# Optimization experiments

Hardware: AMD Instinct MI355X
Metric: run time of the kernel (lower is better)

The kernel has to match this reference:

```python
import jax, jax.numpy as jnp
import numpy as np

B, S, H, HKV, D, BS = 2, 2048, 32, 8, 128, 16
HIDDEN = H * D            # 4096
G = H // HKV              # 4 query heads per kv head
NB = S // BS              # 128 blocks per sequence
SCALE = D ** -0.5


def setup_inputs() -> dict:
    key = jax.random.key(0)
    k1, k2, k3 = jax.random.split(key, 3)
    T = B * S
    hidden_states = jax.random.normal(k1, (T, HIDDEN), dtype=jnp.float32)
    w_qkv = jax.random.normal(k2, (HIDDEN, HIDDEN + 2 * HKV * D), dtype=jnp.float32) * 0.02
    w_out = jax.random.normal(k3, (HIDDEN, HIDDEN), dtype=jnp.float32) * 0.02
    k_cache = jnp.zeros((B * NB, HKV, BS, D), dtype=jnp.float32)
    v_cache = jnp.zeros((B * NB, HKV, BS, D), dtype=jnp.float32)
    block_tables = jnp.arange(B * NB, dtype=jnp.int32).reshape(B, NB)
    return {"hidden_states": hidden_states, "w_qkv": w_qkv, "w_out": w_out,
            "k_cache": k_cache, "v_cache": v_cache, "block_tables": block_tables}


def reference(hidden_states, w_qkv, w_out, k_cache, v_cache, block_tables):
    # qkv projection on packed tokens [T, hidden]
    qkv = hidden_states @ w_qkv
    q, k, v = jnp.split(qkv, [HIDDEN, HIDDEN + HKV * D], axis=-1)
    q = q.reshape(B, S, H, D)
    k = k.reshape(B, S, HKV, D)
    v = v.reshape(B, S, HKV, D)

    # --- paged KV store: scatter per-block pages into cache via block_tables ---
    # [B, NB, BS, HKV, D] -> page layout [B, NB, HKV, BS, D]
    k_pages = k.reshape(B, NB, BS, HKV, D).transpose(0, 1, 3, 2, 4)
    v_pages = v.reshape(B, NB, BS, HKV, D).transpose(0, 1, 3, 2, 4)
    k_cache = k_cache.at[block_tables].set(k_pages)
    v_cache = v_cache.at[block_tables].set(v_pages)

    # --- paged KV gather for prefill attention ---
    kg = k_cache[block_tables].transpose(0, 2, 1, 3, 4).reshape(B, HKV, S, D)
    vg = v_cache[block_tables].transpose(0, 2, 1, 3, 4).reshape(B, HKV, S, D)

    # GQA causal attention: group query heads per kv head
    qh = q.transpose(0, 2, 1, 3).reshape(B, HKV, G, S, D)
    scores = jnp.einsum('bhgqd,bhkd->bhgqk', qh, kg) * SCALE
    causal = jnp.tril(jnp.ones((S, S), dtype=bool))
    scores = jnp.where(causal, scores, -jnp.inf)
    attn = jax.nn.softmax(scores, axis=-1)
    out = jnp.einsum('bhgqk,bhkd->bhgqd', attn, vg)   # [B,HKV,G,S,D]
    out = out.reshape(B, H, S, D).transpose(0, 2, 1, 3).reshape(B * S, HIDDEN)
    return out @ w_out
```

## Files before the change

### kernel.cpp

```cpp
#include <hip/hip_runtime.h>

#define BB 2
#define SS 2048
#define HH 32
#define HKV 8
#define DD 128
#define HIDDEN 4096
#define NQK 6144
#define TT 4096
#define SCALE 0.08838834764831843f
#define SCALE_LOG2E 0.12751743444f

typedef __attribute__((ext_vector_type(8), __may_alias__)) short short8;
typedef __attribute__((ext_vector_type(4), __may_alias__)) short short4v;
typedef __attribute__((ext_vector_type(4), __may_alias__)) float floatx4;

__device__ __forceinline__ short f2bf(float x) {
    unsigned u = __builtin_bit_cast(unsigned, x);
    u += 0x7FFFu + ((u >> 16) & 1u);
    return (short)(u >> 16);
}

__device__ __forceinline__ void gload_lds16(const short* g, short* l) {
    __builtin_amdgcn_global_load_lds((const __attribute__((address_space(1))) void*)g,
                                     (__attribute__((address_space(3))) void*)l, 16, 0, 0);
}

__global__ __launch_bounds__(256) void cvt_f32_bf16(const float* __restrict__ src,
                                                    short* __restrict__ dst) {
    int i = blockIdx.x * 256 + threadIdx.x;
    typedef __attribute__((ext_vector_type(4), __may_alias__)) float f4;
    f4 v = ((const f4*)src)[i];
    short4v o = { f2bf(v.x), f2bf(v.y), f2bf(v.z), f2bf(v.w) };
    ((short4v*)dst)[i] = o;
}

__global__ __launch_bounds__(256) void transpose_cvt(const float* __restrict__ src,
                                                     short* __restrict__ dst,
                                                     int rows, int cols) {
    __shared__ float t[32][33];
    int tx = threadIdx.x, ty = threadIdx.y;
    int c0 = blockIdx.x * 32, r0 = blockIdx.y * 32;
#pragma unroll
    for (int i = 0; i < 32; i += 8) t[ty + i][tx] = src[(size_t)(r0 + ty + i) * cols + c0 + tx];
    __syncthreads();
#pragma unroll
    for (int i = 0; i < 32; i += 8)
        dst[(size_t)(c0 + ty + i) * rows + r0 + tx] = f2bf(t[tx][ty + i]);
}

__global__ __launch_bounds__(256) void build_vt(const short* __restrict__ qkv,
                                                short* __restrict__ vt) {
    __shared__ short t[32][33];
    int tx = threadIdx.x, ty = threadIdx.y;
    int s0 = blockIdx.x * 32, d0 = blockIdx.y * 32;
    int bh = blockIdx.z; int b = bh >> 3, hk = bh & 7;
#pragma unroll
    for (int i = 0; i < 32; i += 8)
        t[ty + i][tx] = qkv[(size_t)(b * SS + s0 + ty + i) * NQK + 5120 + hk * DD + d0 + tx];
    __syncthreads();
#pragma unroll
    for (int i = 0; i < 32; i += 8)
        vt[(size_t)(bh * DD + d0 + ty + i) * SS + s0 + tx] = t[tx][ty + i];
}

template <int OUT_BF16>
__global__ __launch_bounds__(512, 2) void gemm_bt(const short* __restrict__ A,
                                                  const short* __restrict__ Bt,
                                                  void* __restrict__ Cout,
                                                  int M, int N, int K) {
    (void)M;
    __shared__ __align__(16) short smem[65536];
    const int tid  = threadIdx.x;
    const int wave = tid >> 6, lane = tid & 63;
    const int qn = lane & 15, quad = lane >> 4;
    const int wm = wave >> 2, wn = wave & 3;

    int bid = blockIdx.y * gridDim.x + blockIdx.x;
    int xcd = bid & 7, idx = bid >> 3;
    int bnx = gridDim.x >> 2;
    int xm = xcd & 1, xn = xcd >> 1;
    int im = idx & 7, in_ = idx >> 3;
    const int m0 = (xm * 8 + im) * 256;
    const int n0 = (xn * bnx + in_) * 256;

    const int NT = K >> 6;

    const int srow = tid >> 3;
    const int scg  = (tid & 7) ^ (srow & 7);
    const short* aS = A  + (size_t)(m0 + srow) * K + scg * 8;
    const short* bS = Bt + (size_t)(n0 + srow) * K + scg * 8;
    const int lwo = wave * 512;

#define STAGE_A(buf, blk, tt) gload_lds16(aS + (size_t)(blk) * 64 * K + (size_t)(tt) * 64, \
                                          smem + (buf) + (blk) * 4096 + lwo)
#define STAGE_B(buf, blk, tt) gload_lds16(bS + (size_t)(blk) * 64 * K + (size_t)(tt) * 64, \
                                          smem + (buf) + 16384 + (blk) * 4096 + lwo)

    const int xorm  = (qn & 7) << 3;
    const int a_row = (wm * 128 + qn) * 64;
    const int b_row = (wn * 64 + qn) * 64;
    const int col0  = (quad * 8) ^ xorm;
    const int col1  = col0 ^ 32;

#pragma unroll
    for (int blk = 0; blk < 4; blk++) { STAGE_A(0, blk, 0); STAGE_B(0, blk, 0); }
    if (NT > 1) {
#pragma unroll
        for (int blk = 0; blk < 4; blk++) { STAGE_A(32768, blk, 1); STAGE_B(32768, blk, 1); }
        asm volatile("s_waitcnt vmcnt(8)" ::: "memory");
    } else {
        asm volatile("s_waitcnt vmcnt(0)" ::: "memory");
    }
    __builtin_amdgcn_s_barrier();

    floatx4 acc[8][4] = {};

#pragma unroll 2
    for (int t = 0; t < NT; ++t) {
        const int cb = (t & 1) << 15;
        const short* Ab = smem + cb;
        const short* Bb = smem + cb + 16384;
        short8 a[4][2], b0[2][2], b1[2][2], a2[4][2];

#pragma unroll
        for (int mt = 0; mt < 4; mt++) {
            a[mt][0] = *(const short8*)(Ab + a_row + mt * 1024 + col0);
            a[mt][1] = *(const short8*)(Ab + a_row + mt * 1024 + col1);
        }
#pragma unroll
        for (int nt = 0; nt < 2; nt++) {
            b0[nt][0] = *(const short8*)(Bb + b_row + nt * 1024 + col0);
            b0[nt][1] = *(const short8*)(Bb + b_row + nt * 1024 + col1);
        }
        asm volatile("s_waitcnt lgkmcnt(8)" ::: "memory");
        __builtin_amdgcn_s_barrier();
        asm volatile("s_waitcnt lgkmcnt(0)" ::: "memory");
        __builtin_amdgcn_s_setprio(1);
#pragma unroll
        for (int mt = 0; mt < 4; mt++)
#pragma unroll
            for (int nt = 0; nt < 2; nt++) {
                acc[mt][nt] = __builtin_amdgcn_mfma_f32_16x16x32_bf16(a[mt][0], b0[nt][0], acc[mt][nt], 0, 0, 0);
                acc[mt][nt] = __builtin_amdgcn_mfma_f32_16x16x32_bf16(a[mt][1], b0[nt][1], acc[mt][nt], 0, 0, 0);
            }
        __builtin_amdgcn_s_setprio(0);
        __builtin_amdgcn_s_barrier();

#pragma unroll
        for (int nt = 0; nt < 2; nt++) {
            b1[nt][0] = *(const short8*)(Bb + b_row + 2048 + nt * 1024 + col0);
            b1[nt][1] = *(const short8*)(Bb + b_row + 2048 + nt * 1024 + col1);
        }
        if (t + 2 < NT) { STAGE_A(cb, 0, t + 2); STAGE_A(cb, 2, t + 2); }
        __builtin_amdgcn_s_barrier();
        asm volatile("s_waitcnt lgkmcnt(0)" ::: "memory");
        __builtin_amdgcn_s_setprio(1);
#pragma unroll
        for (int mt = 0; mt < 4; mt++)
#pragma unroll
            for (int nt = 0; nt < 2; nt++) {
                acc[mt][2 + nt] = __builtin_amdgcn_mfma_f32_16x16x32_bf16(a[mt][0], b1[nt][0], acc[mt][2 + nt], 0, 0, 0);
                acc[mt][2 + nt] = __builtin_amdgcn_mfma_f32_16x16x32_bf16(a[mt][1], b1[nt][1], acc[mt][2 + nt], 0, 0, 0);
            }
        __builtin_amdgcn_s_setprio(0);
        __builtin_amdgcn_s_barrier();

#pragma unroll
        for (int mt = 0; mt < 4; mt++) {
            a2[mt][0] = *(const short8*)(Ab + 4096 + a_row + mt * 1024 + col0);
            a2[mt][1] = *(const short8*)(Ab + 4096 + a_row + mt * 1024 + col1);
        }
        if (t + 2 < NT) { STAGE_B(cb, 0, t + 2); STAGE_B(cb, 1, t + 2);
                          STAGE_B(cb, 2, t + 2); STAGE_B(cb, 3, t + 2); }
        __builtin_amdgcn_s_barrier();
        asm volatile("s_waitcnt lgkmcnt(0)" ::: "memory");
        __builtin_amdgcn_s_setprio(1);
#pragma unroll
        for (int mt = 0; mt < 4; mt++)
#pragma unroll
            for (int nt = 0; nt < 2; nt++) {
                acc[4 + mt][2 + nt] = __builtin_amdgcn_mfma_f32_16x16x32_bf16(a2[mt][0], b1[nt][0], acc[4 + mt][2 + nt], 0, 0, 0);
                acc[4 + mt][2 + nt] = __builtin_amdgcn_mfma_f32_16x16x32_bf16(a2[mt][1], b1[nt][1], acc[4 + mt][2 + nt], 0, 0, 0);
            }
        __builtin_amdgcn_s_setprio(0);
        __builtin_amdgcn_s_barrier();

        if (t + 2 < NT) { STAGE_A(cb, 1, t + 2); STAGE_A(cb, 3, t + 2); }
        __builtin_amdgcn_s_setprio(1);
#pragma unroll
        for (int mt = 0; mt < 4; mt++)
#pragma unroll
            for (int nt = 0; nt < 2; nt++) {
                acc[4 + mt][nt] = __builtin_amdgcn_mfma_f32_16x16x32_bf16(a2[mt][0], b0[nt][0], acc[4 + mt][nt], 0, 0, 0);
                acc[4 + mt][nt] = __builtin_amdgcn_mfma_f32_16x16x32_bf16(a2[mt][1], b0[nt][1], acc[4 + mt][nt], 0, 0, 0);
            }
        __builtin_amdgcn_s_setprio(0);
        if (t + 2 < NT) asm volatile("s_waitcnt vmcnt(8)" ::: "memory");
        else            asm volatile("s_waitcnt vmcnt(0)" ::: "memory");
        __builtin_amdgcn_s_barrier();
    }
#undef STAGE_A
#undef STAGE_B

    const int erow = m0 + wm * 128 + quad * 4;
    const int ecol = n0 + wn * 64 + qn;
#pragma unroll
    for (int mt = 0; mt < 8; mt++)
#pragma unroll
        for (int nt = 0; nt < 4; nt++)
#pragma unroll
            for (int r = 0; r < 4; r++) {
                size_t off = (size_t)(erow + mt * 16 + r) * N + ecol + nt * 16;
                if (OUT_BF16) ((short*)Cout)[off] = f2bf(acc[mt][nt][r]);
                else          ((float*)Cout)[off] = acc[mt][nt][r];
            }
}

__global__ __launch_bounds__(256) void attn_kernel(const short* __restrict__ qkv,
                                                   const short* __restrict__ vt,
                                                   short* __restrict__ out) {
    __shared__ __align__(16) short Kb[2 * 64 * 128];
    __shared__ __align__(16) short Vb[2 * 128 * 64];
    __shared__ __align__(16) short Ps[4 * 32 * 40];
    int tid = threadIdx.x, wave = tid >> 6, lane = tid & 63;
    int qn = lane & 15, quad = lane >> 4;
    int bid = blockIdx.x;
    int qt = 63 - (bid >> 4);
    int b  = (bid >> 3) & 1;
    int hk = bid & 7;
    int qb = qt * 32;
    int h  = hk * 4 + wave;
    int bh = b * 8 + hk;

    short8 qf[2][4];
#pragma unroll
    for (int nt = 0; nt < 2; nt++) {
        const short* qrow = qkv + (size_t)(b * SS + qb + nt * 16 + qn) * NQK + h * DD;
#pragma unroll
        for (int c = 0; c < 4; c++) qf[nt][c] = *(const short8*)(qrow + c * 32 + quad * 8);
    }
    const short8 onesv = { 0x3F80, 0x3F80, 0x3F80, 0x3F80, 0x3F80, 0x3F80, 0x3F80, 0x3F80 };
    floatx4 oacc[8][2] = {};
    floatx4 lacc[2] = {};
    const int nmac = (qt + 2) >> 1;

    const int kRow = tid >> 4;
    const int kCgp = (tid & 15) ^ (kRow & 7);
    const int vRow = tid >> 3;
    const int vCgp = (tid & 7) ^ (vRow & 7);
    const short* kSrc = qkv + (size_t)(b * SS) * NQK + HIDDEN + hk * DD + kCgp * 8;
    const short* vSrc = vt + (size_t)(bh * DD) * SS + vCgp * 8;
    short* kDst = Kb + wave * 512;
    short* vDst = Vb + wave * 512;

#define STAGEKV(buf, kb) do {                                                          \
    _Pragma("unroll")                                                                  \
    for (int c = 0; c < 4; c++)                                                        \
        gload_lds16(kSrc + (size_t)((kb) + c * 16 + kRow) * NQK,                       \
                    kDst + (buf) * 8192 + c * 2048);                                   \
    _Pragma("unroll")                                                                  \
    for (int c = 0; c < 4; c++)                                                        \
        gload_lds16(vSrc + (size_t)(c * 32 + vRow) * SS + (kb),                        \
                    vDst + (buf) * 8192 + c * 2048);                                   \
    } while (0)

    STAGEKV(0, 0);
    __syncthreads();

    const int kxor = (qn & 7) * 8;

    for (int it = 0; it < nmac; ++it) {
        const int cur = it & 1;
        if (it + 1 < nmac) STAGEKV(cur ^ 1, (it + 1) * 64);
        const short* Kc = Kb + cur * 8192;
        const short* Vc = Vb + cur * 8192;

#pragma unroll
        for (int s = 0; s < 2; ++s) {
            const int kb_s = it * 64 + s * 32;
            if (kb_s > qb) break;
            const bool needMask = (kb_s == qb);

            floatx4 sc[2][2] = {};
#pragma unroll
            for (int c = 0; c < 4; c++) {
                int cg = ((c * 4 + quad) * 8) ^ kxor;
                short8 k0 = *(const short8*)(Kc + (s * 32 + qn) * 128 + cg);
                short8 k1 = *(const short8*)(Kc + (s * 32 + 16 + qn) * 128 + cg);
#pragma unroll
                for (int nt = 0; nt < 2; nt++) {
                    sc[0][nt] = __builtin_amdgcn_mfma_f32_16x16x32_bf16(k0, qf[nt][c], sc[0][nt], 0, 0, 0);
                    sc[1][nt] = __builtin_amdgcn_mfma_f32_16x16x32_bf16(k1, qf[nt][c], sc[1][nt], 0, 0, 0);
                }
            }

            short* pw = Ps + wave * (32 * 40);
#pragma unroll
            for (int nt = 0; nt < 2; nt++)
#pragma unroll
                for (int kt = 0; kt < 2; kt++) {
                    float e[4];
#pragma unroll
                    for (int r = 0; r < 4; r++) {
                        float v = exp2f(sc[kt][nt][r] * SCALE_LOG2E);
                        bool masked = needMask && (kb_s + kt * 16 + quad * 4 + r > qb + nt * 16 + qn);
                        e[r] = masked ? 0.f : v;
                    }
                    short4v pk = { f2bf(e[0]), f2bf(e[1]), f2bf(e[2]), f2bf(e[3]) };
                    *(short4v*)(pw + (nt * 16 + qn) * 40 + kt * 16 + quad * 4) = pk;
                }
            short8 pf[2];
#pragma unroll
            for (int nt = 0; nt < 2; nt++)
                pf[nt] = *(const short8*)(pw + (nt * 16 + qn) * 40 + quad * 8);

            __builtin_amdgcn_s_setprio(1);
#pragma unroll
            for (int dt = 0; dt < 8; dt++) {
                short8 vf = *(const short8*)(Vc + (dt * 16 + qn) * 64 + ((((s << 2) + quad) * 8) ^ kxor));
#pragma unroll
                for (int nt = 0; nt < 2; nt++)
                    oacc[dt][nt] = __builtin_amdgcn_mfma_f32_16x16x32_bf16(vf, pf[nt], oacc[dt][nt], 0, 0, 0);
            }
#pragma unroll
            for (int nt = 0; nt < 2; nt++)
                lacc[nt] = __builtin_amdgcn_mfma_f32_16x16x32_bf16(onesv, pf[nt], lacc[nt], 0, 0, 0);
            __builtin_amdgcn_s_setprio(0);
        }
        __syncthreads();
    }
#undef STAGEKV

#pragma unroll
    for (int nt = 0; nt < 2; nt++) {
        float inv = 1.0f / lacc[nt][0];
        short* orow = out + (size_t)(b * SS + qb + nt * 16 + qn) * HIDDEN + h * DD;
#pragma unroll
        for (int dt = 0; dt < 8; dt++) {
            short4v ov = { f2bf(oacc[dt][nt][0] * inv), f2bf(oacc[dt][nt][1] * inv),
                           f2bf(oacc[dt][nt][2] * inv), f2bf(oacc[dt][nt][3] * inv) };
            *(short4v*)(orow + dt * 16 + quad * 4) = ov;
        }
    }
}

extern "C" void kernel_launch(void* const* d_in, const int* in_sizes, int n_in,
                              void* d_out, int out_size, void* d_ws, size_t ws_size,
                              hipStream_t stream) {
    (void)in_sizes; (void)n_in; (void)out_size; (void)ws_size;
    const float* hs    = (const float*)d_in[0];
    const float* w_qkv = (const float*)d_in[1];
    const float* w_out = (const float*)d_in[2];

    char* ws = (char*)d_ws;
    short* hsb   = (short*)(ws);
    short* wqkvT = (short*)(ws + 33554432);
    short* woutT = (short*)(ws + 83886080);
    short* qkv   = (short*)(ws + 117440512);
    short* vtb   = (short*)(ws + 167772160);
    short* attnb = (short*)(ws + 176160768);

    cvt_f32_bf16<<<16384, 256, 0, stream>>>(hs, hsb);
    transpose_cvt<<<dim3(192, 128), dim3(32, 8), 0, stream>>>(w_qkv, wqkvT, HIDDEN, NQK);
    transpose_cvt<<<dim3(128, 128), dim3(32, 8), 0, stream>>>(w_out, woutT, HIDDEN, HIDDEN);
    gemm_bt<1><<<dim3(NQK / 256, TT / 256), 512, 0, stream>>>(hsb, wqkvT, qkv, TT, NQK, HIDDEN);
    build_vt<<<dim3(64, 4, 16), dim3(32, 8), 0, stream>>>(qkv, vtb);
    attn_kernel<<<1024, 256, 0, stream>>>(qkv, vtb, attnb);
    gemm_bt<0><<<dim3(HIDDEN / 256, TT / 256), 512, 0, stream>>>(attnb, woutT, d_out, TT, HIDDEN, HIDDEN);
}
```

Before: 734.7 us.

## Split attention query rows across 8 waves and vectorize weight transpose

The attention kernel now launches 512 threads per block. Each wave handles 16 query rows of one head instead of 32, so there are 8 waves. KV tiles shrink from 64 to 32 keys, each tile is staged with one LDS load per thread, and the swizzle is reworked to match. The goal is more waves per CU and fewer live registers per wave, at the cost of more barrier iterations over a smaller tile. Separately, the weight transpose-convert kernel uses 64x64 tiles with float4 loads and 16-byte bf16 stores to cut memory transactions.

```diff
diff --git a/kernel.cpp b/kernel.cpp
--- a/kernel.cpp
+++ b/kernel.cpp
@@ -14,6 +14,7 @@
 typedef __attribute__((ext_vector_type(8), __may_alias__)) short short8;
 typedef __attribute__((ext_vector_type(4), __may_alias__)) short short4v;
 typedef __attribute__((ext_vector_type(4), __may_alias__)) float floatx4;
+typedef __attribute__((ext_vector_type(4), __may_alias__)) float f4;
 
 __device__ __forceinline__ short f2bf(float x) {
     unsigned u = __builtin_bit_cast(unsigned, x);
@@ -29,7 +30,6 @@
 __global__ __launch_bounds__(256) void cvt_f32_bf16(const float* __restrict__ src,
                                                     short* __restrict__ dst) {
     int i = blockIdx.x * 256 + threadIdx.x;
-    typedef __attribute__((ext_vector_type(4), __may_alias__)) float f4;
     f4 v = ((const f4*)src)[i];
     short4v o = { f2bf(v.x), f2bf(v.y), f2bf(v.z), f2bf(v.w) };
     ((short4v*)dst)[i] = o;
@@ -38,15 +38,27 @@
 __global__ __launch_bounds__(256) void transpose_cvt(const float* __restrict__ src,
                                                      short* __restrict__ dst,
                                                      int rows, int cols) {
-    __shared__ float t[32][33];
-    int tx = threadIdx.x, ty = threadIdx.y;
-    int c0 = blockIdx.x * 32, r0 = blockIdx.y * 32;
-#pragma unroll
-    for (int i = 0; i < 32; i += 8) t[ty + i][tx] = src[(size_t)(r0 + ty + i) * cols + c0 + tx];
+    __shared__ float t[64][65];
+    int c0 = blockIdx.x * 64, r0 = blockIdx.y * 64;
+    int tx = threadIdx.x & 15, ty = threadIdx.x >> 4;
+#pragma unroll
+    for (int i = 0; i < 64; i += 16) {
+        f4 v = *(const f4*)(src + (size_t)(r0 + ty + i) * cols + c0 + tx * 4);
+        t[ty + i][tx * 4 + 0] = v.x;
+        t[ty + i][tx * 4 + 1] = v.y;
+        t[ty + i][tx * 4 + 2] = v.z;
+        t[ty + i][tx * 4 + 3] = v.w;
+    }
     __syncthreads();
-#pragma unroll
-    for (int i = 0; i < 32; i += 8)
-        dst[(size_t)(c0 + ty + i) * rows + r0 + tx] = f2bf(t[tx][ty + i]);
+    int ox = threadIdx.x & 7, oy = threadIdx.x >> 3;
+#pragma unroll
+    for (int i = 0; i < 64; i += 32) {
+        int cc = oy + i;
+        short8 s;
+#pragma unroll
+        for (int j = 0; j < 8; j++) s[j] = f2bf(t[ox * 8 + j][cc]);
+        *(short8*)(dst + (size_t)(c0 + cc) * rows + r0 + ox * 8) = s;
+    }
 }
 
 __global__ __launch_bounds__(256) void build_vt(const short* __restrict__ qkv,
@@ -217,12 +229,12 @@
             }
 }
 
-__global__ __launch_bounds__(256) void attn_kernel(const short* __restrict__ qkv,
-                                                   const short* __restrict__ vt,
-                                                   short* __restrict__ out) {
-    __shared__ __align__(16) short Kb[2 * 64 * 128];
-    __shared__ __align__(16) short Vb[2 * 128 * 64];
-    __shared__ __align__(16) short Ps[4 * 32 * 40];
+__global__ __launch_bounds__(512, 4) void attn_kernel(const short* __restrict__ qkv,
+                                                      const short* __restrict__ vt,
+                                                      short* __restrict__ out) {
+    __shared__ __align__(16) short Kb[2 * 32 * 128];
+    __shared__ __align__(16) short Vb[2 * 128 * 32];
+    __shared__ __align__(16) short Ps[8 * 16 * 40];
     int tid = threadIdx.x, wave = tid >> 6, lane = tid & 63;
     int qn = lane & 15, quad = lane >> 4;
     int bid = blockIdx.x;
@@ -230,118 +242,92 @@
     int b  = (bid >> 3) & 1;
     int hk = bid & 7;
     int qb = qt * 32;
-    int h  = hk * 4 + wave;
+    int qh = wave >> 2;
+    int h  = hk * 4 + (wave & 3);
     int bh = b * 8 + hk;
-
-    short8 qf[2][4];
-#pragma unroll
-    for (int nt = 0; nt < 2; nt++) {
-        const short* qrow = qkv + (size_t)(b * SS + qb + nt * 16 + qn) * NQK + h * DD;
-#pragma unroll
-        for (int c = 0; c < 4; c++) qf[nt][c] = *(const short8*)(qrow + c * 32 + quad * 8);
+    int rowq = qb + qh * 16 + qn;
+
+    short8 qf[4];
+    {
+        const short* qrow = qkv + (size_t)(b * SS + rowq) * NQK + h * DD;
+#pragma unroll
+        for (int c = 0; c < 4; c++) qf[c] = *(const short8*)(qrow + c * 32 + quad * 8);
     }
     const short8 onesv = { 0x3F80, 0x3F80, 0x3F80, 0x3F80, 0x3F80, 0x3F80, 0x3F80, 0x3F80 };
-    floatx4 oacc[8][2] = {};
-    floatx4 lacc[2] = {};
-    const int nmac = (qt + 2) >> 1;
+    floatx4 oacc[8] = {};
+    floatx4 lacc = {};
+    const int ntiles = qt + 1;
 
     const int kRow = tid >> 4;
     const int kCgp = (tid & 15) ^ (kRow & 7);
-    const int vRow = tid >> 3;
-    const int vCgp = (tid & 7) ^ (vRow & 7);
+    const int vRow = tid >> 2;
+    const int vCgp = (tid & 3) ^ ((vRow >> 1) & 3);
     const short* kSrc = qkv + (size_t)(b * SS) * NQK + HIDDEN + hk * DD + kCgp * 8;
     const short* vSrc = vt + (size_t)(bh * DD) * SS + vCgp * 8;
     short* kDst = Kb + wave * 512;
     short* vDst = Vb + wave * 512;
 
-#define STAGEKV(buf, kb) do {                                                          \
-    _Pragma("unroll")                                                                  \
-    for (int c = 0; c < 4; c++)                                                        \
-        gload_lds16(kSrc + (size_t)((kb) + c * 16 + kRow) * NQK,                       \
-                    kDst + (buf) * 8192 + c * 2048);                                   \
-    _Pragma("unroll")                                                                  \
-    for (int c = 0; c < 4; c++)                                                        \
-        gload_lds16(vSrc + (size_t)(c * 32 + vRow) * SS + (kb),                        \
-                    vDst + (buf) * 8192 + c * 2048);                                   \
+#define STAGEKV(buf, kb) do {                                                   \
+        gload_lds16(kSrc + (size_t)((kb) + kRow) * NQK, kDst + (buf) * 4096);   \
+        gload_lds16(vSrc + (size_t)vRow * SS + (kb),    vDst + (buf) * 4096);   \
     } while (0)
 
     STAGEKV(0, 0);
     __syncthreads();
 
-    const int kxor = (qn & 7) * 8;
-
-    for (int it = 0; it < nmac; ++it) {
+    short* pw = Ps + wave * (16 * 40);
+    for (int it = 0; it < ntiles; ++it) {
+        const int kb = it * 32;
         const int cur = it & 1;
-        if (it + 1 < nmac) STAGEKV(cur ^ 1, (it + 1) * 64);
-        const short* Kc = Kb + cur * 8192;
-        const short* Vc = Vb + cur * 8192;
-
-#pragma unroll
-        for (int s = 0; s < 2; ++s) {
-            const int kb_s = it * 64 + s * 32;
-            if (kb_s > qb) break;
-            const bool needMask = (kb_s == qb);
-
-            floatx4 sc[2][2] = {};
-#pragma unroll
-            for (int c = 0; c < 4; c++) {
-                int cg = ((c * 4 + quad) * 8) ^ kxor;
-                short8 k0 = *(const short8*)(Kc + (s * 32 + qn) * 128 + cg);
-                short8 k1 = *(const short8*)(Kc + (s * 32 + 16 + qn) * 128 + cg);
-#pragma unroll
-                for (int nt = 0; nt < 2; nt++) {
-                    sc[0][nt] = __builtin_amdgcn_mfma_f32_16x16x32_bf16(k0, qf[nt][c], sc[0][nt], 0, 0, 0);
-                    sc[1][nt] = __builtin_amdgcn_mfma_f32_16x16x32_bf16(k1, qf[nt][c], sc[1][nt], 0, 0, 0);
-                }
-            }
-
-            short* pw = Ps + wave * (32 * 40);
-#pragma unroll
-            for (int nt = 0; nt < 2; nt++)
-#pragma unroll
-                for (int kt = 0; kt < 2; kt++) {
-                    float e[4];
-#pragma unroll
-                    for (int r = 0; r < 4; r++) {
-                        float v = exp2f(sc[kt][nt][r] * SCALE_LOG2E);
-                        bool masked = needMask && (kb_s + kt * 16 + quad * 4 + r > qb + nt * 16 + qn);
-                        e[r] = masked ? 0.f : v;
-                    }
-                    short4v pk = { f2bf(e[0]), f2bf(e[1]), f2bf(e[2]), f2bf(e[3]) };
-                    *(short4v*)(pw + (nt * 16 + qn) * 40 + kt * 16 + quad * 4) = pk;
-                }
-            short8 pf[2];
-#pragma unroll
-            for (int nt = 0; nt < 2; nt++)
-                pf[nt] = *(const short8*)(pw + (nt * 16 + qn) * 40 + quad * 8);
-
-            __builtin_amdgcn_s_setprio(1);
-#pragma unroll
-            for (int dt = 0; dt < 8; dt++) {
-                short8 vf = *(const short8*)(Vc + (dt * 16 + qn) * 64 + ((((s << 2) + quad) * 8) ^ kxor));
-#pragma unroll
-                for (int nt = 0; nt < 2; nt++)
-                    oacc[dt][nt] = __builtin_amdgcn_mfma_f32_16x16x32_bf16(vf, pf[nt], oacc[dt][nt], 0, 0, 0);
-            }
-#pragma unroll
-            for (int nt = 0; nt < 2; nt++)
-                lacc[nt] = __builtin_amdgcn_mfma_f32_16x16x32_bf16(onesv, pf[nt], lacc[nt], 0, 0, 0);
-            __builtin_amdgcn_s_setprio(0);
-        }
+        if (it + 1 < ntiles) STAGEKV(cur ^ 1, kb + 32);
+        const short* Kc = Kb + cur * 4096;
+        const short* Vc = Vb + cur * 4096;
+
+        floatx4 sc[2] = {};
+#pragma unroll
+        for (int c = 0; c < 4; c++) {
+            int cg = (((c * 4 + quad) ^ (qn & 7)) * 8);
+            short8 k0 = *(const short8*)(Kc + qn * 128 + cg);
+            short8 k1 = *(const short8*)(Kc + (16 + qn) * 128 + cg);
+            sc[0] = __builtin_amdgcn_mfma_f32_16x16x32_bf16(k0, qf[c], sc[0], 0, 0, 0);
+            sc[1] = __builtin_amdgcn_mfma_f32_16x16x32_bf16(k1, qf[c], sc[1], 0, 0, 0);
+        }
+
+        const bool needMask = (kb + 31 > qb + qh * 16);
+#pragma unroll
+        for (int kt = 0; kt < 2; kt++) {
+            float e[4];
+#pragma unroll
+            for (int r = 0; r < 4; r++) {
+                float v = exp2f(sc[kt][r] * SCALE_LOG2E);
+                bool masked = needMask && (kb + kt * 16 + quad * 4 + r > rowq);
+                e[r] = masked ? 0.f : v;
+            }
+            short4v pk = { f2bf(e[0]), f2bf(e[1]), f2bf(e[2]), f2bf(e[3]) };
+            *(short4v*)(pw + qn * 40 + kt * 16 + quad * 4) = pk;
+        }
+        short8 pf = *(const short8*)(pw + qn * 40 + quad * 8);
+
+        __builtin_amdgcn_s_setprio(1);
+#pragma unroll
+        for (int dt = 0; dt < 8; dt++) {
+            int vg = ((quad ^ ((qn >> 1) & 3)) * 8);
+            short8 vf = *(const short8*)(Vc + (dt * 16 + qn) * 32 + vg);
+            oacc[dt] = __builtin_amdgcn_mfma_f32_16x16x32_bf16(vf, pf, oacc[dt], 0, 0, 0);
+        }
+        lacc = __builtin_amdgcn_mfma_f32_16x16x32_bf16(onesv, pf, lacc, 0, 0, 0);
+        __builtin_amdgcn_s_setprio(0);
         __syncthreads();
     }
 #undef STAGEKV
 
-#pragma unroll
-    for (int nt = 0; nt < 2; nt++) {
-        float inv = 1.0f / lacc[nt][0];
-        short* orow = out + (size_t)(b * SS + qb + nt * 16 + qn) * HIDDEN + h * DD;
-#pragma unroll
-        for (int dt = 0; dt < 8; dt++) {
-            short4v ov = { f2bf(oacc[dt][nt][0] * inv), f2bf(oacc[dt][nt][1] * inv),
-                           f2bf(oacc[dt][nt][2] * inv), f2bf(oacc[dt][nt][3] * inv) };
-            *(short4v*)(orow + dt * 16 + quad * 4) = ov;
-        }
+    float inv = 1.0f / lacc[0];
+    short* orow = out + (size_t)(b * SS + rowq) * HIDDEN + h * DD;
+#pragma unroll
+    for (int dt = 0; dt < 8; dt++) {
+        short4v ov = { f2bf(oacc[dt][0] * inv), f2bf(oacc[dt][1] * inv),
+                       f2bf(oacc[dt][2] * inv), f2bf(oacc[dt][3] * inv) };
+        *(short4v*)(orow + dt * 16 + quad * 4) = ov;
     }
 }
 
@@ -362,10 +348,10 @@
     short* attnb = (short*)(ws + 176160768);
 
     cvt_f32_bf16<<<16384, 256, 0, stream>>>(hs, hsb);
-    transpose_cvt<<<dim3(192, 128), dim3(32, 8), 0, stream>>>(w_qkv, wqkvT, HIDDEN, NQK);
-    transpose_cvt<<<dim3(128, 128), dim3(32, 8), 0, stream>>>(w_out, woutT, HIDDEN, HIDDEN);
+    transpose_cvt<<<dim3(NQK / 64, HIDDEN / 64), 256, 0, stream>>>(w_qkv, wqkvT, HIDDEN, NQK);
+    transpose_cvt<<<dim3(HIDDEN / 64, HIDDEN / 64), 256, 0, stream>>>(w_out, woutT, HIDDEN, HIDDEN);
     gemm_bt<1><<<dim3(NQK / 256, TT / 256), 512, 0, stream>>>(hsb, wqkvT, qkv, TT, NQK, HIDDEN);
     build_vt<<<dim3(64, 4, 16), dim3(32, 8), 0, stream>>>(qkv, vtb);
-    attn_kernel<<<1024, 256, 0, stream>>>(qkv, vtb, attnb);
+    attn_kernel<<<1024, 512, 0, stream>>>(qkv, vtb, attnb);
     gemm_bt<0><<<dim3(HIDDEN / 256, TT / 256), 512, 0, stream>>>(attnb, woutT, d_out, TT, HIDDEN, HIDDEN);
 }
```

After: 712.3 us. 3.0% less time.
